# Kernel optimization log

Hardware: AMD Instinct MI355X
Metric: run time of the kernel (lower is better)

## Reference

```python
import jax, jax.numpy as jnp
import numpy as np

EPS = 1e-6
SLIDING_WINDOW = 512
SCALING = 256.0 ** -0.5  # query_pre_attn_scalar ** -0.5


def rmsnorm(x, w):
    rms = jnp.sqrt(jnp.mean(jnp.square(x), axis=-1, keepdims=True) + EPS)
    return (x / rms) * (1.0 + w)


def apply_rope(x, cos, sin):
    # x: [B,S,H,D]; cos/sin: [S,D//2] -> pairs of adjacent dims rotated as complex
    B, S, H, D = x.shape
    xr = x.reshape(B, S, H, D // 2, 2)
    a, b = xr[..., 0], xr[..., 1]
    c = cos[None, :, None, :]
    s = sin[None, :, None, :]
    out = jnp.stack([a * c - b * s, a * s + b * c], axis=-1)
    return out.reshape(B, S, H, D)


def setup_inputs() -> dict:
    key = jax.random.key(0)
    ks = jax.random.split(key, 8)
    B, S, E, H, D = 2, 4096, 640, 4, 256
    x = jax.random.normal(ks[0], (B, S, E), dtype=jnp.float32)
    # RoPE tables (rope_local_base=10000 for sliding layers)
    inv_freq = 1.0 / (10000.0 ** (np.arange(0, D, 2, dtype=np.float32) / D))
    t = np.arange(S, dtype=np.float32)
    freqs = np.outer(t, inv_freq)  # [S, D//2]
    cos = jnp.asarray(np.cos(freqs), dtype=jnp.float32)
    sin = jnp.asarray(np.sin(freqs), dtype=jnp.float32)
    sc = 1.0 / np.sqrt(E)
    Wq = jax.random.normal(ks[1], (E, H * D), dtype=jnp.float32) * sc
    Wk = jax.random.normal(ks[2], (E, 1 * D), dtype=jnp.float32) * sc
    Wv = jax.random.normal(ks[3], (E, 1 * D), dtype=jnp.float32) * sc
    Wo = jax.random.normal(ks[4], (H * D, E), dtype=jnp.float32) * (1.0 / np.sqrt(H * D))
    q_norm_w = jnp.zeros((D,), dtype=jnp.float32)  # torch init: zeros, acts as weight 1+0
    k_norm_w = jnp.zeros((D,), dtype=jnp.float32)
    return {"x": x, "cos": cos, "sin": sin, "Wq": Wq, "Wk": Wk, "Wv": Wv,
            "Wo": Wo, "q_norm_w": q_norm_w, "k_norm_w": k_norm_w}


def reference(x, cos, sin, Wq, Wk, Wv, Wo, q_norm_w, k_norm_w):
    B, S, E = x.shape
    H, D = 4, 256
    q = (x @ Wq).reshape(B, S, H, D)
    k = (x @ Wk).reshape(B, S, 1, D)
    v = (x @ Wv).reshape(B, S, 1, D)
    q = rmsnorm(q, q_norm_w)
    k = rmsnorm(k, k_norm_w)
    q = apply_rope(q, cos, sin)
    k = apply_rope(k, cos, sin)
    k0 = k[:, :, 0, :]  # [B,S,D] single KV head (MQA)
    v0 = v[:, :, 0, :]
    scores = jnp.einsum('bqhd,bkd->bhqk', q, k0) * SCALING  # [B,H,S,S]
    i = jnp.arange(S)[:, None]
    j = jnp.arange(S)[None, :]
    # causal AND within sliding window: 0 <= i-j <= W
    allowed = (j <= i) & (i - j <= SLIDING_WINDOW)
    scores = jnp.where(allowed[None, None], scores, -jnp.inf)
    attn = jax.nn.softmax(scores, axis=-1)
    out = jnp.einsum('bhqk,bkd->bqhd', attn, v0).reshape(B, S, H * D)
    return out @ Wo
```

## Files before the change

kernel.cpp:

```cpp
#include <hip/hip_runtime.h>
#include <hip/hip_bf16.h>

#define S_LEN 4096
#define NH 4
#define HD 256
#define WIN 512
#define ATT_SCALE 0.0625f
#define QKV_N 1536

typedef short s16x8 __attribute__((ext_vector_type(8)));
typedef float f32x4 __attribute__((ext_vector_type(4)));

static __device__ inline unsigned short f2bf(float f) {
  union { float f; unsigned int u; } v; v.f = f;
  unsigned int r = v.u + 0x7fff + ((v.u >> 16) & 1);
  return (unsigned short)(r >> 16);
}
static __device__ inline float bf2f(unsigned short h) {
  union { unsigned int u; float f; } v; v.u = ((unsigned int)h) << 16;
  return v.f;
}
static __device__ inline void gl2lds16(const void* g, void* l) {
  __builtin_amdgcn_global_load_lds(
      (const __attribute__((address_space(1))) unsigned int*)g,
      (__attribute__((address_space(3))) unsigned int*)l, 16, 0, 0);
}

static __device__ void trcast_tile(const float* __restrict__ src,
                                   unsigned short* __restrict__ dst,
                                   int K, int N, int bn, int bk, int tid,
                                   float* ts ) {
#pragma unroll
  for (int it = 0; it < 4; ++it) {
    const int c = it * 256 + tid;
    const int row = c >> 4, col4 = (c & 15) << 2;
    const float4 v = *(const float4*)(src + (size_t)(bk * 64 + row) * N + bn * 64 + col4);
    ts[row * 65 + col4 + 0] = v.x; ts[row * 65 + col4 + 1] = v.y;
    ts[row * 65 + col4 + 2] = v.z; ts[row * 65 + col4 + 3] = v.w;
  }
  __syncthreads();
#pragma unroll
  for (int it = 0; it < 4; ++it) {
    const int c = it * 256 + tid;
    const int nrow = c >> 4, kc4 = (c & 15) << 2;
    const unsigned int p0 = f2bf(ts[(kc4 + 0) * 65 + nrow]) | ((unsigned int)f2bf(ts[(kc4 + 1) * 65 + nrow]) << 16);
    const unsigned int p1 = f2bf(ts[(kc4 + 2) * 65 + nrow]) | ((unsigned int)f2bf(ts[(kc4 + 3) * 65 + nrow]) << 16);
    *(uint2*)(dst + (size_t)(bn * 64 + nrow) * K + bk * 64 + kc4) = make_uint2(p0, p1);
  }
}

__global__ __launch_bounds__(256) void prep_kernel(
    const float* __restrict__ x, unsigned short* __restrict__ xb,
    const float* __restrict__ Wq, const float* __restrict__ Wk,
    const float* __restrict__ Wv, const float* __restrict__ Wo,
    unsigned short* __restrict__ Wqkvt, unsigned short* __restrict__ Wot) {
  __shared__ float ts[64 * 65];
  const int g = blockIdx.x;
  const int tid = threadIdx.x;
  if (g < 5120) {
    const int t = g * 256 + tid;
    const float4 v = ((const float4*)x)[t];
    const unsigned int p0 = f2bf(v.x) | ((unsigned int)f2bf(v.y) << 16);
    const unsigned int p1 = f2bf(v.z) | ((unsigned int)f2bf(v.w) << 16);
    *(uint2*)(xb + (size_t)t * 4) = make_uint2(p0, p1);
  } else if (g < 5280) {
    const int g2 = g - 5120;
    trcast_tile(Wq, Wqkvt, 640, 1024, g2 & 15, g2 >> 4, tid, ts);
  } else if (g < 5320) {
    const int g2 = g - 5280;
    trcast_tile(Wk, Wqkvt + (size_t)1024 * 640, 640, 256, g2 & 3, g2 >> 2, tid, ts);
  } else if (g < 5360) {
    const int g2 = g - 5320;
    trcast_tile(Wv, Wqkvt + (size_t)1280 * 640, 640, 256, g2 & 3, g2 >> 2, tid, ts);
  } else {
    const int g2 = g - 5360;
    trcast_tile(Wo, Wot, 1024, 640, g2 % 10, g2 / 10, tid, ts);
  }
}

template <bool BF16OUT>
__global__ __launch_bounds__(256) void gemm_bt(const unsigned short* __restrict__ A,
                                               const unsigned short* __restrict__ Bt,
                                               void* __restrict__ Cv,
                                               int M, int N, int K) {
  __shared__ unsigned short As[128 * 32];
  __shared__ unsigned short Bs[128 * 32];
  const int tid = threadIdx.x;
  const int wave = tid >> 6, lane = tid & 63;
  const int ln15 = lane & 15, lgr = lane >> 4;
  const int bm = blockIdx.y, bn = blockIdx.x;
  const int wr = wave & 1, wc = wave >> 1;
  const unsigned short* Ab = A + (size_t)bm * 128 * K;
  const unsigned short* Bb = Bt + (size_t)bn * 128 * K;

  f32x4 acc[4][4];
#pragma unroll
  for (int mt = 0; mt < 4; ++mt)
#pragma unroll
    for (int nt = 0; nt < 4; ++nt) acc[mt][nt] = (f32x4){0.f, 0.f, 0.f, 0.f};

  for (int kt = 0; kt < K; kt += 32) {
#pragma unroll
    for (int i = 0; i < 2; ++i) {
      const int c = tid + 256 * i;
      const int row = c >> 2, kc = (c & 3) << 3;
      gl2lds16(Ab + (size_t)row * K + kt + kc, &As[c * 8]);
      gl2lds16(Bb + (size_t)row * K + kt + kc, &Bs[c * 8]);
    }
    __syncthreads();
    s16x8 af[4], bfr[4];
#pragma unroll
    for (int t = 0; t < 4; ++t) {
      af[t]  = *(const s16x8*)&As[(wr * 64 + t * 16 + ln15) * 32 + lgr * 8];
      bfr[t] = *(const s16x8*)&Bs[(wc * 64 + t * 16 + ln15) * 32 + lgr * 8];
    }
#pragma unroll
    for (int mt = 0; mt < 4; ++mt)
#pragma unroll
      for (int nt = 0; nt < 4; ++nt)
        acc[mt][nt] = __builtin_amdgcn_mfma_f32_16x16x32_bf16(af[mt], bfr[nt], acc[mt][nt], 0, 0, 0);
    __syncthreads();
  }

#pragma unroll
  for (int mt = 0; mt < 4; ++mt)
#pragma unroll
    for (int nt = 0; nt < 4; ++nt)
#pragma unroll
      for (int r = 0; r < 4; ++r) {
        const size_t row = bm * 128 + wr * 64 + mt * 16 + lgr * 4 + r;
        const size_t col = bn * 128 + wc * 64 + nt * 16 + ln15;
        if (BF16OUT) ((unsigned short*)Cv)[row * N + col] = f2bf(acc[mt][nt][r]);
        else         ((float*)Cv)[row * N + col] = acc[mt][nt][r];
      }
}

__global__ __launch_bounds__(256) void gemm_bt64(const unsigned short* __restrict__ A,
                                                 const unsigned short* __restrict__ Bt,
                                                 float* __restrict__ C,
                                                 int M, int N, int K) {
  __shared__ unsigned short As[64 * 32];
  __shared__ unsigned short Bs[128 * 32];
  const int tid = threadIdx.x;
  const int wave = tid >> 6, lane = tid & 63;
  const int ln15 = lane & 15, lgr = lane >> 4;
  const int bm = blockIdx.y, bn = blockIdx.x;
  const unsigned short* Ab = A + (size_t)bm * 64 * K;
  const unsigned short* Bb = Bt + (size_t)bn * 128 * K;

  f32x4 acc[4][2];
#pragma unroll
  for (int mt = 0; mt < 4; ++mt)
#pragma unroll
    for (int nt = 0; nt < 2; ++nt) acc[mt][nt] = (f32x4){0.f, 0.f, 0.f, 0.f};

  for (int kt = 0; kt < K; kt += 32) {
    {
      const int row = tid >> 2, kc = (tid & 3) << 3;
      gl2lds16(Ab + (size_t)row * K + kt + kc, &As[tid * 8]);
#pragma unroll
      for (int i = 0; i < 2; ++i) {
        const int c = tid + 256 * i;
        const int brow = c >> 2, bkc = (c & 3) << 3;
        gl2lds16(Bb + (size_t)brow * K + kt + bkc, &Bs[c * 8]);
      }
    }
    __syncthreads();
    s16x8 af[4], bfr[2];
#pragma unroll
    for (int t = 0; t < 4; ++t)
      af[t] = *(const s16x8*)&As[(t * 16 + ln15) * 32 + lgr * 8];
#pragma unroll
    for (int t = 0; t < 2; ++t)
      bfr[t] = *(const s16x8*)&Bs[(wave * 32 + t * 16 + ln15) * 32 + lgr * 8];
#pragma unroll
    for (int mt = 0; mt < 4; ++mt)
#pragma unroll
      for (int nt = 0; nt < 2; ++nt)
        acc[mt][nt] = __builtin_amdgcn_mfma_f32_16x16x32_bf16(af[mt], bfr[nt], acc[mt][nt], 0, 0, 0);
    __syncthreads();
  }

#pragma unroll
  for (int mt = 0; mt < 4; ++mt)
#pragma unroll
    for (int nt = 0; nt < 2; ++nt)
#pragma unroll
      for (int r = 0; r < 4; ++r) {
        const size_t row = bm * 64 + mt * 16 + lgr * 4 + r;
        const size_t col = bn * 128 + wave * 32 + nt * 16 + ln15;
        C[row * N + col] = acc[mt][nt][r];
      }
}

__global__ __launch_bounds__(256) void normrope_vt_kernel(
    unsigned short* __restrict__ qkv,
    const float* __restrict__ cosb, const float* __restrict__ sinb,
    const float* __restrict__ qw, const float* __restrict__ kw,
    unsigned short* __restrict__ vtb) {
  const int idx = blockIdx.x;
  const int tid = threadIdx.x;
  if (idx < 40960) {
    const int h = idx % 5;
    const int bs = idx / 5;
    const int s = bs & (S_LEN - 1);
    unsigned short* base = qkv + (size_t)bs * QKV_N;
    unsigned short* row; const float* w; float oscale;
    if (h < 4) { row = base + h * HD;  w = qw; oscale = ATT_SCALE; }
    else       { row = base + 4 * HD;  w = kw; oscale = 1.0f; }
    const int lane = tid & 63, wave = tid >> 6;
    __shared__ float xs[HD];
    __shared__ float red[4];
    const float xv = bf2f(row[tid]);
    xs[tid] = xv;
    float ssq = xv * xv;
#pragma unroll
    for (int off = 32; off > 0; off >>= 1) ssq += __shfl_xor(ssq, off);
    if (lane == 0) red[wave] = ssq;
    __syncthreads();
    const float tot = red[0] + red[1] + red[2] + red[3];
    const float inv = rsqrtf(tot * (1.0f / 256.0f) + 1e-6f);
    const int pi = tid >> 1;
    const float c = cosb[s * (HD / 2) + pi];
    const float sn = sinb[s * (HD / 2) + pi];
    const float a = xs[pi * 2]     * inv * (1.0f + w[pi * 2]);
    const float b = xs[pi * 2 + 1] * inv * (1.0f + w[pi * 2 + 1]);
    const float outv = ((tid & 1) ? (a * sn + b * c) : (a * c - b * sn)) * oscale;
    row[tid] = f2bf(outv);
  } else {
    __shared__ unsigned short ts[32][264];
    const int g2 = idx - 40960;
    const int b = g2 >> 7, jt = g2 & 127;
    const unsigned short* src = qkv + ((size_t)(b * S_LEN) + jt * 32) * QKV_N + 5 * HD;
#pragma unroll
    for (int it = 0; it < 4; ++it) {
      const int c = tid + 256 * it;
      const int row = c >> 5, col8 = (c & 31) << 3;
      *(uint4*)&ts[row][col8] = *(const uint4*)(src + (size_t)row * QKV_N + col8);
    }
    __syncthreads();
    unsigned short tmp[32];
#pragma unroll
    for (int s2 = 0; s2 < 32; ++s2) {
      const int jj = (s2 >> 1) | ((s2 & 1) << 4);
      tmp[s2] = ts[jj][tid];
    }
    unsigned short* dst = vtb + ((size_t)(b * 128 + jt) * 256 + tid) * 32;
#pragma unroll
    for (int wq = 0; wq < 4; ++wq) *(uint4*)(dst + wq * 8) = *(uint4*)(tmp + wq * 8);
  }
}

#define PS_LD 40

__global__ __launch_bounds__(256) void attn_mfma_kernel(
    const unsigned short* __restrict__ qkv, const unsigned short* __restrict__ vtb,
    unsigned short* __restrict__ aob) {
  const int g = blockIdx.x;
  const int xcd = g & 7, slot = g >> 3;
  const int h = slot >> 4;
  const int qt = xcd * 16 + (slot & 15);
  const int b = qt >> 6;
  const int q0 = (qt & 63) << 6;
  const int tid = threadIdx.x;
  const int wave = tid >> 6;
  const int lane = tid & 63;
  const int ln15 = lane & 15;
  const int lgr = lane >> 4;

  __shared__ unsigned short Ks[2][16 * 512];
  __shared__ unsigned short Vts[2][16 * 512];
  __shared__ unsigned short Ps[4][16 * PS_LD];

  const size_t qrow = (size_t)(b * S_LEN + q0 + wave * 16 + ln15) * QKV_N + h * HD;
  s16x8 qfrag[8];
#pragma unroll
  for (int f = 0; f < 8; ++f)
    qfrag[f] = *(const s16x8*)(qkv + qrow + f * 32 + lgr * 8);

  f32x4 acc[16];
#pragma unroll
  for (int t = 0; t < 16; ++t) acc[t] = (f32x4){0.f, 0.f, 0.f, 0.f};
  float l_part[4] = {0.f, 0.f, 0.f, 0.f};

  const int kt_lo = max(0, q0 - WIN) >> 5;
  const int kt_hi = (q0 + 63) >> 5;
  const unsigned short* kbase = qkv + (size_t)(b * S_LEN) * QKV_N + 4 * HD;
  const unsigned short* vbase = vtb + (size_t)b * (S_LEN / 32) * HD * 32;

  auto stage = [&](int kt, int buf) {
#pragma unroll
    for (int u = 0; u < 4; ++u) {
      const int c = wave * 4 + u;
      const int ct = c >> 3, f = c & 7;
      const unsigned short* gk =
          kbase + (size_t)(kt * 32 + ct * 16 + ln15) * QKV_N + f * 32 + lgr * 8;
      gl2lds16(gk, &Ks[buf][c * 512]);
      const unsigned short* gv =
          vbase + (size_t)kt * (HD * 32) + (size_t)(c * 16 + ln15) * 32 + lgr * 8;
      gl2lds16(gv, &Vts[buf][c * 512]);
    }
  };

  stage(kt_lo, 0);
  __syncthreads();

  unsigned short* psw = Ps[wave];
  const int i_row0 = q0 + wave * 16 + lgr * 4;

  for (int kt = kt_lo; kt <= kt_hi; ++kt) {
    const int cur = (kt - kt_lo) & 1;
    if (kt < kt_hi) stage(kt + 1, cur ^ 1);

    f32x4 sc[2];
    sc[0] = (f32x4){0.f, 0.f, 0.f, 0.f};
    sc[1] = (f32x4){0.f, 0.f, 0.f, 0.f};
#pragma unroll
    for (int f = 0; f < 8; ++f) {
#pragma unroll
      for (int ct = 0; ct < 2; ++ct) {
        const s16x8 kf = *(const s16x8*)&Ks[cur][(ct * 8 + f) * 512 + lane * 8];
        sc[ct] = __builtin_amdgcn_mfma_f32_16x16x32_bf16(qfrag[f], kf, sc[ct], 0, 0, 0);
      }
    }

    const int j0 = kt * 32 + ln15;
    float p0[4], p1[4];
#pragma unroll
    for (int r = 0; r < 4; ++r) {
      const int i = i_row0 + r;
      const bool a0 = (j0 <= i) && (i - j0 <= WIN);
      const bool a1 = (j0 + 16 <= i) && (i - (j0 + 16) <= WIN);
      const float e0 = __expf(sc[0][r] - 16.0f);
      const float e1 = __expf(sc[1][r] - 16.0f);
      p0[r] = a0 ? e0 : 0.0f;
      p1[r] = a1 ? e1 : 0.0f;
      l_part[r] += p0[r] + p1[r];
    }
#pragma unroll
    for (int r = 0; r < 4; ++r) {
      const unsigned int pk = (unsigned int)f2bf(p0[r]) | ((unsigned int)f2bf(p1[r]) << 16);
      *(unsigned int*)&psw[(lgr * 4 + r) * PS_LD + (ln15 << 1)] = pk;
    }
    const s16x8 pf = *(const s16x8*)&psw[ln15 * PS_LD + lgr * 8];
#pragma unroll
    for (int t = 0; t < 16; ++t) {
      const s16x8 vf = *(const s16x8*)&Vts[cur][t * 512 + lane * 8];
      acc[t] = __builtin_amdgcn_mfma_f32_16x16x32_bf16(pf, vf, acc[t], 0, 0, 0);
    }
    __syncthreads();
  }

#pragma unroll
  for (int off = 1; off < 16; off <<= 1)
#pragma unroll
    for (int r = 0; r < 4; ++r) l_part[r] += __shfl_xor(l_part[r], off);

  float inv_l[4];
#pragma unroll
  for (int r = 0; r < 4; ++r) inv_l[r] = 1.0f / l_part[r];
#pragma unroll
  for (int t = 0; t < 16; ++t)
#pragma unroll
    for (int r = 0; r < 4; ++r) {
      const size_t orow = (size_t)(b * S_LEN + q0 + wave * 16 + lgr * 4 + r);
      aob[(orow * NH + h) * HD + t * 16 + ln15] = f2bf(acc[t][r] * inv_l[r]);
    }
}

extern "C" void kernel_launch(void* const* d_in, const int* in_sizes, int n_in,
                              void* d_out, int out_size, void* d_ws, size_t ws_size,
                              hipStream_t stream) {
  const float* x    = (const float*)d_in[0];
  const float* cosb = (const float*)d_in[1];
  const float* sinb = (const float*)d_in[2];
  const float* Wq   = (const float*)d_in[3];
  const float* Wk   = (const float*)d_in[4];
  const float* Wv   = (const float*)d_in[5];
  const float* Wo   = (const float*)d_in[6];
  const float* qw   = (const float*)d_in[7];
  const float* kw   = (const float*)d_in[8];
  float* out = (float*)d_out;

  unsigned short* ws = (unsigned short*)d_ws;
  unsigned short* xb     = ws;
  unsigned short* Wqkvt  = xb + 5242880;
  unsigned short* Wot    = Wqkvt + 983040;
  unsigned short* qkvb   = Wot + 655360;
  unsigned short* vtb    = qkvb + 12582912;
  unsigned short* aob    = vtb + 2097152;
  const int M = 2 * S_LEN;

  prep_kernel<<<5520, 256, 0, stream>>>(x, xb, Wq, Wk, Wv, Wo, Wqkvt, Wot);
  gemm_bt<true><<<dim3(QKV_N / 128, M / 128), 256, 0, stream>>>(xb, Wqkvt, qkvb, M, QKV_N, 640);
  normrope_vt_kernel<<<M * 5 + 256, 256, 0, stream>>>(qkvb, cosb, sinb, qw, kw, vtb);
  attn_mfma_kernel<<<M / 64 * NH, 256, 0, stream>>>(qkvb, vtb, aob);
  gemm_bt64<<<dim3(640 / 128, M / 64), 256, 0, stream>>>(aob, Wot, out, M, 640, 1024);
}
```

Before: 215.4 us.

## Double per-wave query rows in attention to reuse K/V tiles across two subtiles

The attention kernel now gives each block 128 query rows instead of 64, with each wave handling two 16-row subtiles that share every staged K and V fragment. This halves the grid to 256 blocks and amortizes K/V global-to-LDS traffic and LDS fragment reads over twice the MFMA work. In exchange, per-thread accumulator registers double, so launch bounds are set to one block per CU, which lowers occupancy. With only 256 blocks on a 256-CU part, there is also less parallel slack for load balancing.

```diff
diff --git a/kernel.cpp b/kernel.cpp
--- a/kernel.cpp
+++ b/kernel.cpp
@@ -253,15 +253,15 @@
 
 #define PS_LD 40
 
-__global__ __launch_bounds__(256) void attn_mfma_kernel(
+__global__ __launch_bounds__(256, 1) void attn_mfma_kernel(
     const unsigned short* __restrict__ qkv, const unsigned short* __restrict__ vtb,
     unsigned short* __restrict__ aob) {
   const int g = blockIdx.x;
   const int xcd = g & 7, slot = g >> 3;
-  const int h = slot >> 4;
-  const int qt = xcd * 16 + (slot & 15);
-  const int b = qt >> 6;
-  const int q0 = (qt & 63) << 6;
+  const int h = slot >> 3;
+  const int qt = xcd * 8 + (slot & 7);
+  const int b = qt >> 5;
+  const int q0 = (qt & 31) << 7;
   const int tid = threadIdx.x;
   const int wave = tid >> 6;
   const int lane = tid & 63;
@@ -270,21 +270,27 @@
 
   __shared__ unsigned short Ks[2][16 * 512];
   __shared__ unsigned short Vts[2][16 * 512];
-  __shared__ unsigned short Ps[4][16 * PS_LD];
-
-  const size_t qrow = (size_t)(b * S_LEN + q0 + wave * 16 + ln15) * QKV_N + h * HD;
-  s16x8 qfrag[8];
-#pragma unroll
-  for (int f = 0; f < 8; ++f)
-    qfrag[f] = *(const s16x8*)(qkv + qrow + f * 32 + lgr * 8);
-
-  f32x4 acc[16];
-#pragma unroll
-  for (int t = 0; t < 16; ++t) acc[t] = (f32x4){0.f, 0.f, 0.f, 0.f};
-  float l_part[4] = {0.f, 0.f, 0.f, 0.f};
+  __shared__ unsigned short Ps[4][2][16 * PS_LD];
+
+  s16x8 qfrag[2][8];
+#pragma unroll
+  for (int s = 0; s < 2; ++s) {
+    const size_t qrow =
+        (size_t)(b * S_LEN + q0 + wave * 32 + s * 16 + ln15) * QKV_N + h * HD;
+#pragma unroll
+    for (int f = 0; f < 8; ++f)
+      qfrag[s][f] = *(const s16x8*)(qkv + qrow + f * 32 + lgr * 8);
+  }
+
+  f32x4 acc[2][16];
+#pragma unroll
+  for (int s = 0; s < 2; ++s)
+#pragma unroll
+    for (int t = 0; t < 16; ++t) acc[s][t] = (f32x4){0.f, 0.f, 0.f, 0.f};
+  float l_part[2][4] = {{0.f, 0.f, 0.f, 0.f}, {0.f, 0.f, 0.f, 0.f}};
 
   const int kt_lo = max(0, q0 - WIN) >> 5;
-  const int kt_hi = (q0 + 63) >> 5;
+  const int kt_hi = (q0 + 127) >> 5;
   const unsigned short* kbase = qkv + (size_t)(b * S_LEN) * QKV_N + 4 * HD;
   const unsigned short* vbase = vtb + (size_t)b * (S_LEN / 32) * HD * 32;
 
@@ -305,48 +311,51 @@
   stage(kt_lo, 0);
   __syncthreads();
 
-  unsigned short* psw = Ps[wave];
-  const int i_row0 = q0 + wave * 16 + lgr * 4;
-
   for (int kt = kt_lo; kt <= kt_hi; ++kt) {
     const int cur = (kt - kt_lo) & 1;
     if (kt < kt_hi) stage(kt + 1, cur ^ 1);
 
-    f32x4 sc[2];
-    sc[0] = (f32x4){0.f, 0.f, 0.f, 0.f};
-    sc[1] = (f32x4){0.f, 0.f, 0.f, 0.f};
+    f32x4 sc[2][2];
+#pragma unroll
+    for (int s = 0; s < 2; ++s)
+#pragma unroll
+      for (int ct = 0; ct < 2; ++ct) sc[s][ct] = (f32x4){0.f, 0.f, 0.f, 0.f};
 #pragma unroll
     for (int f = 0; f < 8; ++f) {
 #pragma unroll
       for (int ct = 0; ct < 2; ++ct) {
         const s16x8 kf = *(const s16x8*)&Ks[cur][(ct * 8 + f) * 512 + lane * 8];
-        sc[ct] = __builtin_amdgcn_mfma_f32_16x16x32_bf16(qfrag[f], kf, sc[ct], 0, 0, 0);
+        sc[0][ct] = __builtin_amdgcn_mfma_f32_16x16x32_bf16(qfrag[0][f], kf, sc[0][ct], 0, 0, 0);
+        sc[1][ct] = __builtin_amdgcn_mfma_f32_16x16x32_bf16(qfrag[1][f], kf, sc[1][ct], 0, 0, 0);
       }
     }
 
     const int j0 = kt * 32 + ln15;
-    float p0[4], p1[4];
-#pragma unroll
-    for (int r = 0; r < 4; ++r) {
-      const int i = i_row0 + r;
-      const bool a0 = (j0 <= i) && (i - j0 <= WIN);
-      const bool a1 = (j0 + 16 <= i) && (i - (j0 + 16) <= WIN);
-      const float e0 = __expf(sc[0][r] - 16.0f);
-      const float e1 = __expf(sc[1][r] - 16.0f);
-      p0[r] = a0 ? e0 : 0.0f;
-      p1[r] = a1 ? e1 : 0.0f;
-      l_part[r] += p0[r] + p1[r];
-    }
-#pragma unroll
-    for (int r = 0; r < 4; ++r) {
-      const unsigned int pk = (unsigned int)f2bf(p0[r]) | ((unsigned int)f2bf(p1[r]) << 16);
-      *(unsigned int*)&psw[(lgr * 4 + r) * PS_LD + (ln15 << 1)] = pk;
-    }
-    const s16x8 pf = *(const s16x8*)&psw[ln15 * PS_LD + lgr * 8];
+#pragma unroll
+    for (int s = 0; s < 2; ++s) {
+      const int ib = q0 + wave * 32 + s * 16 + lgr * 4;
+      unsigned short* psw = Ps[wave][s];
+#pragma unroll
+      for (int r = 0; r < 4; ++r) {
+        const int i = ib + r;
+        const bool a0 = (j0 <= i) && (i - j0 <= WIN);
+        const bool a1 = (j0 + 16 <= i) && (i - (j0 + 16) <= WIN);
+        const float e0 = __expf(sc[s][0][r] - 16.0f);
+        const float e1 = __expf(sc[s][1][r] - 16.0f);
+        const float p0 = a0 ? e0 : 0.0f;
+        const float p1 = a1 ? e1 : 0.0f;
+        l_part[s][r] += p0 + p1;
+        const unsigned int pk = (unsigned int)f2bf(p0) | ((unsigned int)f2bf(p1) << 16);
+        *(unsigned int*)&psw[(lgr * 4 + r) * PS_LD + (ln15 << 1)] = pk;
+      }
+    }
+    const s16x8 pf0 = *(const s16x8*)&Ps[wave][0][ln15 * PS_LD + lgr * 8];
+    const s16x8 pf1 = *(const s16x8*)&Ps[wave][1][ln15 * PS_LD + lgr * 8];
 #pragma unroll
     for (int t = 0; t < 16; ++t) {
       const s16x8 vf = *(const s16x8*)&Vts[cur][t * 512 + lane * 8];
-      acc[t] = __builtin_amdgcn_mfma_f32_16x16x32_bf16(pf, vf, acc[t], 0, 0, 0);
+      acc[0][t] = __builtin_amdgcn_mfma_f32_16x16x32_bf16(pf0, vf, acc[0][t], 0, 0, 0);
+      acc[1][t] = __builtin_amdgcn_mfma_f32_16x16x32_bf16(pf1, vf, acc[1][t], 0, 0, 0);
     }
     __syncthreads();
   }
@@ -354,18 +363,24 @@
 #pragma unroll
   for (int off = 1; off < 16; off <<= 1)
 #pragma unroll
-    for (int r = 0; r < 4; ++r) l_part[r] += __shfl_xor(l_part[r], off);
-
-  float inv_l[4];
-#pragma unroll
-  for (int r = 0; r < 4; ++r) inv_l[r] = 1.0f / l_part[r];
-#pragma unroll
-  for (int t = 0; t < 16; ++t)
-#pragma unroll
-    for (int r = 0; r < 4; ++r) {
-      const size_t orow = (size_t)(b * S_LEN + q0 + wave * 16 + lgr * 4 + r);
-      aob[(orow * NH + h) * HD + t * 16 + ln15] = f2bf(acc[t][r] * inv_l[r]);
-    }
+    for (int s = 0; s < 2; ++s)
+#pragma unroll
+      for (int r = 0; r < 4; ++r) l_part[s][r] += __shfl_xor(l_part[s][r], off);
+
+#pragma unroll
+  for (int s = 0; s < 2; ++s) {
+    float inv_l[4];
+#pragma unroll
+    for (int r = 0; r < 4; ++r) inv_l[r] = 1.0f / l_part[s][r];
+#pragma unroll
+    for (int t = 0; t < 16; ++t)
+#pragma unroll
+      for (int r = 0; r < 4; ++r) {
+        const size_t orow =
+            (size_t)(b * S_LEN + q0 + wave * 32 + s * 16 + lgr * 4 + r);
+        aob[(orow * NH + h) * HD + t * 16 + ln15] = f2bf(acc[s][t][r] * inv_l[r]);
+      }
+  }
 }
 
 extern "C" void kernel_launch(void* const* d_in, const int* in_sizes, int n_in,
@@ -394,6 +409,6 @@
   prep_kernel<<<5520, 256, 0, stream>>>(x, xb, Wq, Wk, Wv, Wo, Wqkvt, Wot);
   gemm_bt<true><<<dim3(QKV_N / 128, M / 128), 256, 0, stream>>>(xb, Wqkvt, qkvb, M, QKV_N, 640);
   normrope_vt_kernel<<<M * 5 + 256, 256, 0, stream>>>(qkvb, cosb, sinb, qw, kw, vtb);
-  attn_mfma_kernel<<<M / 64 * NH, 256, 0, stream>>>(qkvb, vtb, aob);
+  attn_mfma_kernel<<<256, 256, 0, stream>>>(qkvb, vtb, aob);
   gemm_bt64<<<dim3(640 / 128, M / 64), 256, 0, stream>>>(aob, Wot, out, M, 640, 1024);
 }
```

Result: slower. 231.7 us (+7.6%).

## Fuse RMSNorm, RoPE and V transpose into the QKV GEMM epilogue

Applied to the files above, without the earlier changes.

The QKV projection GEMM now uses 64x256 tiles, so each block holds a full head row. RMSNorm, RoPE and scaling are applied in registers in the epilogue, and V is transposed through LDS into the attention layout, which removes the separate normrope_vt kernel and its round trip of the qkv buffer through memory. Cos and sin are interleaved into a float2 table in the prep kernel, and both GEMMs switch to a per-16-row LDS tile layout for their global-to-LDS loads. The trade-offs are fewer, larger GEMM blocks (768 instead of 768 with 128x128 tiles, but more accumulator registers) and cross-lane shuffles in the epilogue.

```diff
diff --git a/kernel.cpp b/kernel.cpp
--- a/kernel.cpp
+++ b/kernel.cpp
@@ -16,10 +16,6 @@
   unsigned int r = v.u + 0x7fff + ((v.u >> 16) & 1);
   return (unsigned short)(r >> 16);
 }
-static __device__ inline float bf2f(unsigned short h) {
-  union { unsigned int u; float f; } v; v.u = ((unsigned int)h) << 16;
-  return v.f;
-}
 static __device__ inline void gl2lds16(const void* g, void* l) {
   __builtin_amdgcn_global_load_lds(
       (const __attribute__((address_space(1))) unsigned int*)g,
@@ -53,7 +49,9 @@
     const float* __restrict__ x, unsigned short* __restrict__ xb,
     const float* __restrict__ Wq, const float* __restrict__ Wk,
     const float* __restrict__ Wv, const float* __restrict__ Wo,
-    unsigned short* __restrict__ Wqkvt, unsigned short* __restrict__ Wot) {
+    unsigned short* __restrict__ Wqkvt, unsigned short* __restrict__ Wot,
+    const float* __restrict__ cosb, const float* __restrict__ sinb,
+    float2* __restrict__ csb) {
   __shared__ float ts[64 * 65];
   const int g = blockIdx.x;
   const int tid = threadIdx.x;
@@ -72,75 +70,147 @@
   } else if (g < 5360) {
     const int g2 = g - 5320;
     trcast_tile(Wv, Wqkvt + (size_t)1280 * 640, 640, 256, g2 & 3, g2 >> 2, tid, ts);
-  } else {
+  } else if (g < 5520) {
     const int g2 = g - 5360;
     trcast_tile(Wo, Wot, 1024, 640, g2 % 10, g2 / 10, tid, ts);
-  }
-}
-
-template <bool BF16OUT>
-__global__ __launch_bounds__(256) void gemm_bt(const unsigned short* __restrict__ A,
-                                               const unsigned short* __restrict__ Bt,
-                                               void* __restrict__ Cv,
-                                               int M, int N, int K) {
-  __shared__ unsigned short As[128 * 32];
-  __shared__ unsigned short Bs[128 * 32];
+  } else {
+    const int t = (g - 5520) * 256 + tid;
+    csb[t] = make_float2(cosb[t], sinb[t]);
+  }
+}
+
+__global__ __launch_bounds__(256) void gemm_qkv_fused(
+    const unsigned short* __restrict__ A, const unsigned short* __restrict__ Bt,
+    const float2* __restrict__ csb,
+    const float* __restrict__ qw, const float* __restrict__ kw,
+    unsigned short* __restrict__ qkvb, unsigned short* __restrict__ vtb) {
+  __shared__ unsigned short sm[16512];
+  __shared__ float red[64][2];
   const int tid = threadIdx.x;
   const int wave = tid >> 6, lane = tid & 63;
   const int ln15 = lane & 15, lgr = lane >> 4;
-  const int bm = blockIdx.y, bn = blockIdx.x;
+  const int bn = blockIdx.x, bm = blockIdx.y;
   const int wr = wave & 1, wc = wave >> 1;
-  const unsigned short* Ab = A + (size_t)bm * 128 * K;
-  const unsigned short* Bb = Bt + (size_t)bn * 128 * K;
-
-  f32x4 acc[4][4];
-#pragma unroll
-  for (int mt = 0; mt < 4; ++mt)
-#pragma unroll
-    for (int nt = 0; nt < 4; ++nt) acc[mt][nt] = (f32x4){0.f, 0.f, 0.f, 0.f};
-
-  for (int kt = 0; kt < K; kt += 32) {
-#pragma unroll
-    for (int i = 0; i < 2; ++i) {
-      const int c = tid + 256 * i;
-      const int row = c >> 2, kc = (c & 3) << 3;
-      gl2lds16(Ab + (size_t)row * K + kt + kc, &As[c * 8]);
-      gl2lds16(Bb + (size_t)row * K + kt + kc, &Bs[c * 8]);
-    }
-    __syncthreads();
-    s16x8 af[4], bfr[4];
-#pragma unroll
-    for (int t = 0; t < 4; ++t) {
-      af[t]  = *(const s16x8*)&As[(wr * 64 + t * 16 + ln15) * 32 + lgr * 8];
-      bfr[t] = *(const s16x8*)&Bs[(wc * 64 + t * 16 + ln15) * 32 + lgr * 8];
-    }
-#pragma unroll
-    for (int mt = 0; mt < 4; ++mt)
-#pragma unroll
-      for (int nt = 0; nt < 4; ++nt)
+  const int K = 640;
+  const unsigned short* Ab = A + (size_t)bm * 64 * K;
+  const unsigned short* Bb = Bt + (size_t)bn * 256 * K;
+
+  f32x4 acc[2][8];
+#pragma unroll
+  for (int mt = 0; mt < 2; ++mt)
+#pragma unroll
+    for (int nt = 0; nt < 8; ++nt) acc[mt][nt] = (f32x4){0.f, 0.f, 0.f, 0.f};
+
+  for (int kt = 0; kt < 640; kt += 32) {
+#pragma unroll
+    for (int u = 0; u < 5; ++u) {
+      const int c = wave * 5 + u;
+      if (c < 4)
+        gl2lds16(Ab + (size_t)(c * 16 + ln15) * K + kt + lgr * 8, &sm[c * 512]);
+      else
+        gl2lds16(Bb + (size_t)((c - 4) * 16 + ln15) * K + kt + lgr * 8, &sm[c * 512]);
+    }
+    __syncthreads();
+    s16x8 af[2], bfr[8];
+#pragma unroll
+    for (int mt = 0; mt < 2; ++mt)
+      af[mt] = *(const s16x8*)&sm[(wr * 2 + mt) * 512 + lane * 8];
+#pragma unroll
+    for (int nt = 0; nt < 8; ++nt)
+      bfr[nt] = *(const s16x8*)&sm[(4 + wc * 8 + nt) * 512 + lane * 8];
+#pragma unroll
+    for (int mt = 0; mt < 2; ++mt)
+#pragma unroll
+      for (int nt = 0; nt < 8; ++nt)
         acc[mt][nt] = __builtin_amdgcn_mfma_f32_16x16x32_bf16(af[mt], bfr[nt], acc[mt][nt], 0, 0, 0);
     __syncthreads();
   }
 
-#pragma unroll
-  for (int mt = 0; mt < 4; ++mt)
-#pragma unroll
-    for (int nt = 0; nt < 4; ++nt)
+  if (bn < 5) {
+    const float* w = (bn < 4) ? qw : kw;
+    const float scale = (bn < 4) ? ATT_SCALE : 1.0f;
+    float part[2][4];
+#pragma unroll
+    for (int mt = 0; mt < 2; ++mt)
 #pragma unroll
       for (int r = 0; r < 4; ++r) {
-        const size_t row = bm * 128 + wr * 64 + mt * 16 + lgr * 4 + r;
-        const size_t col = bn * 128 + wc * 64 + nt * 16 + ln15;
-        if (BF16OUT) ((unsigned short*)Cv)[row * N + col] = f2bf(acc[mt][nt][r]);
-        else         ((float*)Cv)[row * N + col] = acc[mt][nt][r];
+        float s = 0.f;
+#pragma unroll
+        for (int nt = 0; nt < 8; ++nt) s += acc[mt][nt][r] * acc[mt][nt][r];
+        part[mt][r] = s;
       }
+#pragma unroll
+    for (int off = 1; off < 16; off <<= 1)
+#pragma unroll
+      for (int mt = 0; mt < 2; ++mt)
+#pragma unroll
+        for (int r = 0; r < 4; ++r) part[mt][r] += __shfl_xor(part[mt][r], off);
+    if (ln15 == 0) {
+#pragma unroll
+      for (int mt = 0; mt < 2; ++mt)
+#pragma unroll
+        for (int r = 0; r < 4; ++r)
+          red[wr * 32 + mt * 16 + lgr * 4 + r][wc] = part[mt][r];
+    }
+    __syncthreads();
+#pragma unroll
+    for (int mt = 0; mt < 2; ++mt)
+#pragma unroll
+      for (int r = 0; r < 4; ++r) {
+        const int rl = wr * 32 + mt * 16 + lgr * 4 + r;
+        const float inv = rsqrtf((red[rl][0] + red[rl][1]) * (1.0f / 256.0f) + 1e-6f);
+        const int grow = bm * 64 + rl;
+        const int spos = grow & (S_LEN - 1);
+#pragma unroll
+        for (int nt = 0; nt < 8; ++nt) {
+          const int col = wc * 128 + nt * 16 + ln15;
+          const float val = acc[mt][nt][r] * inv * (1.0f + w[col]);
+          const float prt = __shfl_xor(val, 1);
+          const float2 cs = csb[spos * 128 + (col >> 1)];
+          float o = (ln15 & 1) ? (prt * cs.y + val * cs.x)
+                               : (val * cs.x - prt * cs.y);
+          qkvb[(size_t)grow * QKV_N + bn * 256 + col] = f2bf(o * scale);
+        }
+      }
+  } else {
+#pragma unroll
+    for (int mt = 0; mt < 2; ++mt)
+#pragma unroll
+      for (int nt = 0; nt < 8; ++nt)
+#pragma unroll
+        for (int r = 0; r < 4; ++r) {
+          const float val = acc[mt][nt][r];
+          const float prt = __shfl_xor(val, 1);
+          if (!(ln15 & 1)) {
+            const int j = wr * 32 + mt * 16 + lgr * 4 + r;
+            const int d = wc * 128 + nt * 16 + ln15;
+            *(unsigned int*)&sm[j * 258 + d] =
+                (unsigned int)f2bf(val) | ((unsigned int)f2bf(prt) << 16);
+          }
+        }
+    __syncthreads();
+    const int bb = bm >> 6;
+    const int jt0 = (bm & 63) * 2;
+#pragma unroll
+    for (int half = 0; half < 2; ++half) {
+      unsigned short tmp[32];
+#pragma unroll
+      for (int s2 = 0; s2 < 32; ++s2) {
+        const int jj = (s2 >> 1) | ((s2 & 1) << 4);
+        tmp[s2] = sm[(half * 32 + jj) * 258 + tid];
+      }
+      unsigned short* dst = vtb + ((size_t)(bb * 128 + jt0 + half) * 256 + tid) * 32;
+#pragma unroll
+      for (int wq = 0; wq < 4; ++wq) *(uint4*)(dst + wq * 8) = *(uint4*)(tmp + wq * 8);
+    }
+  }
 }
 
 __global__ __launch_bounds__(256) void gemm_bt64(const unsigned short* __restrict__ A,
                                                  const unsigned short* __restrict__ Bt,
                                                  float* __restrict__ C,
                                                  int M, int N, int K) {
-  __shared__ unsigned short As[64 * 32];
-  __shared__ unsigned short Bs[128 * 32];
+  __shared__ unsigned short sm[12 * 512];
   const int tid = threadIdx.x;
   const int wave = tid >> 6, lane = tid & 63;
   const int ln15 = lane & 15, lgr = lane >> 4;
@@ -155,24 +225,22 @@
     for (int nt = 0; nt < 2; ++nt) acc[mt][nt] = (f32x4){0.f, 0.f, 0.f, 0.f};
 
   for (int kt = 0; kt < K; kt += 32) {
-    {
-      const int row = tid >> 2, kc = (tid & 3) << 3;
-      gl2lds16(Ab + (size_t)row * K + kt + kc, &As[tid * 8]);
-#pragma unroll
-      for (int i = 0; i < 2; ++i) {
-        const int c = tid + 256 * i;
-        const int brow = c >> 2, bkc = (c & 3) << 3;
-        gl2lds16(Bb + (size_t)brow * K + kt + bkc, &Bs[c * 8]);
-      }
+#pragma unroll
+    for (int u = 0; u < 3; ++u) {
+      const int c = wave * 3 + u;
+      if (c < 4)
+        gl2lds16(Ab + (size_t)(c * 16 + ln15) * K + kt + lgr * 8, &sm[c * 512]);
+      else
+        gl2lds16(Bb + (size_t)((c - 4) * 16 + ln15) * K + kt + lgr * 8, &sm[c * 512]);
     }
     __syncthreads();
     s16x8 af[4], bfr[2];
 #pragma unroll
     for (int t = 0; t < 4; ++t)
-      af[t] = *(const s16x8*)&As[(t * 16 + ln15) * 32 + lgr * 8];
+      af[t] = *(const s16x8*)&sm[t * 512 + lane * 8];
 #pragma unroll
     for (int t = 0; t < 2; ++t)
-      bfr[t] = *(const s16x8*)&Bs[(wave * 32 + t * 16 + ln15) * 32 + lgr * 8];
+      bfr[t] = *(const s16x8*)&sm[(4 + wave * 2 + t) * 512 + lane * 8];
 #pragma unroll
     for (int mt = 0; mt < 4; ++mt)
 #pragma unroll
@@ -191,64 +259,6 @@
         const size_t col = bn * 128 + wave * 32 + nt * 16 + ln15;
         C[row * N + col] = acc[mt][nt][r];
       }
-}
-
-__global__ __launch_bounds__(256) void normrope_vt_kernel(
-    unsigned short* __restrict__ qkv,
-    const float* __restrict__ cosb, const float* __restrict__ sinb,
-    const float* __restrict__ qw, const float* __restrict__ kw,
-    unsigned short* __restrict__ vtb) {
-  const int idx = blockIdx.x;
-  const int tid = threadIdx.x;
-  if (idx < 40960) {
-    const int h = idx % 5;
-    const int bs = idx / 5;
-    const int s = bs & (S_LEN - 1);
-    unsigned short* base = qkv + (size_t)bs * QKV_N;
-    unsigned short* row; const float* w; float oscale;
-    if (h < 4) { row = base + h * HD;  w = qw; oscale = ATT_SCALE; }
-    else       { row = base + 4 * HD;  w = kw; oscale = 1.0f; }
-    const int lane = tid & 63, wave = tid >> 6;
-    __shared__ float xs[HD];
-    __shared__ float red[4];
-    const float xv = bf2f(row[tid]);
-    xs[tid] = xv;
-    float ssq = xv * xv;
-#pragma unroll
-    for (int off = 32; off > 0; off >>= 1) ssq += __shfl_xor(ssq, off);
-    if (lane == 0) red[wave] = ssq;
-    __syncthreads();
-    const float tot = red[0] + red[1] + red[2] + red[3];
-    const float inv = rsqrtf(tot * (1.0f / 256.0f) + 1e-6f);
-    const int pi = tid >> 1;
-    const float c = cosb[s * (HD / 2) + pi];
-    const float sn = sinb[s * (HD / 2) + pi];
-    const float a = xs[pi * 2]     * inv * (1.0f + w[pi * 2]);
-    const float b = xs[pi * 2 + 1] * inv * (1.0f + w[pi * 2 + 1]);
-    const float outv = ((tid & 1) ? (a * sn + b * c) : (a * c - b * sn)) * oscale;
-    row[tid] = f2bf(outv);
-  } else {
-    __shared__ unsigned short ts[32][264];
-    const int g2 = idx - 40960;
-    const int b = g2 >> 7, jt = g2 & 127;
-    const unsigned short* src = qkv + ((size_t)(b * S_LEN) + jt * 32) * QKV_N + 5 * HD;
-#pragma unroll
-    for (int it = 0; it < 4; ++it) {
-      const int c = tid + 256 * it;
-      const int row = c >> 5, col8 = (c & 31) << 3;
-      *(uint4*)&ts[row][col8] = *(const uint4*)(src + (size_t)row * QKV_N + col8);
-    }
-    __syncthreads();
-    unsigned short tmp[32];
-#pragma unroll
-    for (int s2 = 0; s2 < 32; ++s2) {
-      const int jj = (s2 >> 1) | ((s2 & 1) << 4);
-      tmp[s2] = ts[jj][tid];
-    }
-    unsigned short* dst = vtb + ((size_t)(b * 128 + jt) * 256 + tid) * 32;
-#pragma unroll
-    for (int wq = 0; wq < 4; ++wq) *(uint4*)(dst + wq * 8) = *(uint4*)(tmp + wq * 8);
-  }
 }
 
 #define PS_LD 40
@@ -389,11 +399,13 @@
   unsigned short* qkvb   = Wot + 655360;
   unsigned short* vtb    = qkvb + 12582912;
   unsigned short* aob    = vtb + 2097152;
+  float2* csb = (float2*)aob;
   const int M = 2 * S_LEN;
 
-  prep_kernel<<<5520, 256, 0, stream>>>(x, xb, Wq, Wk, Wv, Wo, Wqkvt, Wot);
-  gemm_bt<true><<<dim3(QKV_N / 128, M / 128), 256, 0, stream>>>(xb, Wqkvt, qkvb, M, QKV_N, 640);
-  normrope_vt_kernel<<<M * 5 + 256, 256, 0, stream>>>(qkvb, cosb, sinb, qw, kw, vtb);
+  prep_kernel<<<7568, 256, 0, stream>>>(x, xb, Wq, Wk, Wv, Wo, Wqkvt, Wot,
+                                        cosb, sinb, csb);
+  gemm_qkv_fused<<<dim3(6, M / 64), 256, 0, stream>>>(xb, Wqkvt, csb, qw, kw,
+                                                      qkvb, vtb);
   attn_mfma_kernel<<<M / 64 * NH, 256, 0, stream>>>(qkvb, vtb, aob);
   gemm_bt64<<<dim3(640 / 128, M / 64), 256, 0, stream>>>(aob, Wot, out, M, 640, 1024);
 }
```

Result: slower. 228.0 us (+5.8%).

## Double-buffer LDS in projection GEMMs and remap blocks for XCD locality

Applied to the files above, without the earlier changes.

Both projection GEMMs now double-buffer their LDS tiles, issuing the next K-slice's global-to-LDS loads before computing the current one. The LDS layout becomes MFMA-fragment order so each lane reads a contiguous 16-byte chunk. Blocks are also remapped so consecutive M tiles land on the same XCD, improving L2 reuse of the A rows. The loop drops its second barrier, which relies on the load path's ordering to avoid overwriting a buffer still being read, and M, N and K are now fixed at compile time.

```diff
diff --git a/kernel.cpp b/kernel.cpp
--- a/kernel.cpp
+++ b/kernel.cpp
@@ -78,17 +78,20 @@
   }
 }
 
-template <bool BF16OUT>
-__global__ __launch_bounds__(256) void gemm_bt(const unsigned short* __restrict__ A,
-                                               const unsigned short* __restrict__ Bt,
-                                               void* __restrict__ Cv,
-                                               int M, int N, int K) {
-  __shared__ unsigned short As[128 * 32];
-  __shared__ unsigned short Bs[128 * 32];
+__global__ __launch_bounds__(256) void gemm_qkv(const unsigned short* __restrict__ A,
+                                                const unsigned short* __restrict__ Bt,
+                                                unsigned short* __restrict__ C) {
+  constexpr int K = 640, N = QKV_N;
+  __shared__ unsigned short As[2][8 * 512];
+  __shared__ unsigned short Bs[2][8 * 512];
+  const int g = blockIdx.x;
+  const int xcd = g & 7;
+  const int i = g >> 3;
+  const int bn = i % 12;
+  const int bm = (i / 12) * 8 + xcd;
   const int tid = threadIdx.x;
   const int wave = tid >> 6, lane = tid & 63;
   const int ln15 = lane & 15, lgr = lane >> 4;
-  const int bm = blockIdx.y, bn = blockIdx.x;
   const int wr = wave & 1, wc = wave >> 1;
   const unsigned short* Ab = A + (size_t)bm * 128 * K;
   const unsigned short* Bb = Bt + (size_t)bn * 128 * K;
@@ -99,20 +102,28 @@
 #pragma unroll
     for (int nt = 0; nt < 4; ++nt) acc[mt][nt] = (f32x4){0.f, 0.f, 0.f, 0.f};
 
-  for (int kt = 0; kt < K; kt += 32) {
-#pragma unroll
-    for (int i = 0; i < 2; ++i) {
-      const int c = tid + 256 * i;
-      const int row = c >> 2, kc = (c & 3) << 3;
-      gl2lds16(Ab + (size_t)row * K + kt + kc, &As[c * 8]);
-      gl2lds16(Bb + (size_t)row * K + kt + kc, &Bs[c * 8]);
-    }
-    __syncthreads();
+  auto stage = [&](int kt, int buf) {
+#pragma unroll
+    for (int u = 0; u < 4; ++u) {
+      const int c = wave * 4 + u;
+      if (c < 8)
+        gl2lds16(Ab + (size_t)(c * 16 + ln15) * K + kt + lgr * 8, &As[buf][c * 512]);
+      else
+        gl2lds16(Bb + (size_t)((c - 8) * 16 + ln15) * K + kt + lgr * 8, &Bs[buf][(c - 8) * 512]);
+    }
+  };
+
+  stage(0, 0);
+  __syncthreads();
+
+  for (int it = 0; it < 20; ++it) {
+    const int cur = it & 1;
+    if (it < 19) stage((it + 1) * 32, cur ^ 1);
     s16x8 af[4], bfr[4];
 #pragma unroll
     for (int t = 0; t < 4; ++t) {
-      af[t]  = *(const s16x8*)&As[(wr * 64 + t * 16 + ln15) * 32 + lgr * 8];
-      bfr[t] = *(const s16x8*)&Bs[(wc * 64 + t * 16 + ln15) * 32 + lgr * 8];
+      af[t]  = *(const s16x8*)&As[cur][(wr * 4 + t) * 512 + lane * 8];
+      bfr[t] = *(const s16x8*)&Bs[cur][(wc * 4 + t) * 512 + lane * 8];
     }
 #pragma unroll
     for (int mt = 0; mt < 4; ++mt)
@@ -130,21 +141,24 @@
       for (int r = 0; r < 4; ++r) {
         const size_t row = bm * 128 + wr * 64 + mt * 16 + lgr * 4 + r;
         const size_t col = bn * 128 + wc * 64 + nt * 16 + ln15;
-        if (BF16OUT) ((unsigned short*)Cv)[row * N + col] = f2bf(acc[mt][nt][r]);
-        else         ((float*)Cv)[row * N + col] = acc[mt][nt][r];
+        C[row * N + col] = f2bf(acc[mt][nt][r]);
       }
 }
 
-__global__ __launch_bounds__(256) void gemm_bt64(const unsigned short* __restrict__ A,
-                                                 const unsigned short* __restrict__ Bt,
-                                                 float* __restrict__ C,
-                                                 int M, int N, int K) {
-  __shared__ unsigned short As[64 * 32];
-  __shared__ unsigned short Bs[128 * 32];
+__global__ __launch_bounds__(256) void gemm_out(const unsigned short* __restrict__ A,
+                                                const unsigned short* __restrict__ Bt,
+                                                float* __restrict__ C) {
+  constexpr int K = 1024, N = 640;
+  __shared__ unsigned short As[2][4 * 512];
+  __shared__ unsigned short Bs[2][8 * 512];
+  const int g = blockIdx.x;
+  const int xcd = g & 7;
+  const int i = g >> 3;
+  const int bn = i % 5;
+  const int bm = (i / 5) * 8 + xcd;
   const int tid = threadIdx.x;
   const int wave = tid >> 6, lane = tid & 63;
   const int ln15 = lane & 15, lgr = lane >> 4;
-  const int bm = blockIdx.y, bn = blockIdx.x;
   const unsigned short* Ab = A + (size_t)bm * 64 * K;
   const unsigned short* Bb = Bt + (size_t)bn * 128 * K;
 
@@ -154,25 +168,30 @@
 #pragma unroll
     for (int nt = 0; nt < 2; ++nt) acc[mt][nt] = (f32x4){0.f, 0.f, 0.f, 0.f};
 
-  for (int kt = 0; kt < K; kt += 32) {
-    {
-      const int row = tid >> 2, kc = (tid & 3) << 3;
-      gl2lds16(Ab + (size_t)row * K + kt + kc, &As[tid * 8]);
-#pragma unroll
-      for (int i = 0; i < 2; ++i) {
-        const int c = tid + 256 * i;
-        const int brow = c >> 2, bkc = (c & 3) << 3;
-        gl2lds16(Bb + (size_t)brow * K + kt + bkc, &Bs[c * 8]);
-      }
-    }
-    __syncthreads();
+  auto stage = [&](int kt, int buf) {
+#pragma unroll
+    for (int u = 0; u < 3; ++u) {
+      const int c = wave * 3 + u;
+      if (c < 4)
+        gl2lds16(Ab + (size_t)(c * 16 + ln15) * K + kt + lgr * 8, &As[buf][c * 512]);
+      else
+        gl2lds16(Bb + (size_t)((c - 4) * 16 + ln15) * K + kt + lgr * 8, &Bs[buf][(c - 4) * 512]);
+    }
+  };
+
+  stage(0, 0);
+  __syncthreads();
+
+  for (int it = 0; it < 32; ++it) {
+    const int cur = it & 1;
+    if (it < 31) stage((it + 1) * 32, cur ^ 1);
     s16x8 af[4], bfr[2];
 #pragma unroll
     for (int t = 0; t < 4; ++t)
-      af[t] = *(const s16x8*)&As[(t * 16 + ln15) * 32 + lgr * 8];
+      af[t] = *(const s16x8*)&As[cur][t * 512 + lane * 8];
 #pragma unroll
     for (int t = 0; t < 2; ++t)
-      bfr[t] = *(const s16x8*)&Bs[(wave * 32 + t * 16 + ln15) * 32 + lgr * 8];
+      bfr[t] = *(const s16x8*)&Bs[cur][(wave * 2 + t) * 512 + lane * 8];
 #pragma unroll
     for (int mt = 0; mt < 4; ++mt)
 #pragma unroll
@@ -392,8 +411,8 @@
   const int M = 2 * S_LEN;
 
   prep_kernel<<<5520, 256, 0, stream>>>(x, xb, Wq, Wk, Wv, Wo, Wqkvt, Wot);
-  gemm_bt<true><<<dim3(QKV_N / 128, M / 128), 256, 0, stream>>>(xb, Wqkvt, qkvb, M, QKV_N, 640);
+  gemm_qkv<<<768, 256, 0, stream>>>(xb, Wqkvt, qkvb);
   normrope_vt_kernel<<<M * 5 + 256, 256, 0, stream>>>(qkvb, cosb, sinb, qw, kw, vtb);
   attn_mfma_kernel<<<M / 64 * NH, 256, 0, stream>>>(qkvb, vtb, aob);
-  gemm_bt64<<<dim3(640 / 128, M / 64), 256, 0, stream>>>(aob, Wot, out, M, 640, 1024);
-}
+  gemm_out<<<640, 256, 0, stream>>>(aob, Wot, out);
+}
```

Result: slower. 231.9 us (+7.6%).
